# Kernel optimization log

Hardware: AMD Instinct MI355X
Metric: run time of the kernel (lower is better)

Reference implementation:

```python
import jax, jax.numpy as jnp
import numpy as np

TEMPERATURE = 1.0
TOP_K = 50
TOP_P = 0.95
NEG_INF = float('-inf')


def setup_inputs() -> dict:
    key = jax.random.key(0)
    k1, k2, k3, k4 = jax.random.split(key, 4)
    B, S, D, V = 32, 8, 1024, 50257
    psi_real = jax.random.normal(k1, (B, S, D), dtype=jnp.float32)
    psi_imag = jax.random.normal(k2, (B, S, D), dtype=jnp.float32)
    W_real = jax.random.normal(k3, (V, D), dtype=jnp.float32) * 0.02
    W_imag = jax.random.normal(k4, (V, D), dtype=jnp.float32) * 0.02
    bias = jnp.zeros((V,), dtype=jnp.float32)
    return {"psi_real": psi_real, "psi_imag": psi_imag, "W_real": W_real,
            "W_imag": W_imag, "bias": bias}


def _legacy_filter(logits, temperature, top_k, top_p):
    # temperature
    l = logits / max(temperature, 1e-8)
    # top-k: keep values >= k-th largest
    if 0 < top_k < l.shape[-1]:
        topk_vals = jax.lax.top_k(l, top_k)[0]          # [B,S,k]
        threshold = topk_vals[..., -1:]
        l = jnp.where(l < threshold, NEG_INF, l)
    # top-p (nucleus): mask tokens where exclusive cumulative prob >= p
    if top_p < 1.0:
        p = max(top_p, 1e-6)
        order = jnp.argsort(-l, axis=-1)                # descending
        sl = jnp.take_along_axis(l, order, axis=-1)
        sp = jax.nn.softmax(sl, axis=-1)
        cum = jnp.cumsum(sp, axis=-1)
        mask = (cum - sp) >= p                          # exclusive cumsum >= p
        mask = mask.at[..., 0].set(False)               # always keep top token
        sl = jnp.where(mask, NEG_INF, sl)
        inv = jnp.argsort(order, axis=-1)               # scatter back to original order
        l = jnp.take_along_axis(sl, inv, axis=-1)
    return l


def reference(psi_real, psi_imag, W_real, W_imag, bias):
    # logits = proj_real(psi.real) + proj_imag(psi.imag) + bias  -> [B,S,V]
    logits = (jnp.einsum('bsd,vd->bsv', psi_real, W_real)
              + jnp.einsum('bsd,vd->bsv', psi_imag, W_imag) + bias)
    sampling_logits = _legacy_filter(logits, TEMPERATURE, TOP_K, TOP_P)
    probs = jax.nn.softmax(sampling_logits, axis=-1)
    # multinomial(probs, 1) == categorical over filtered logits
    tokens = jax.random.categorical(jax.random.key(42), sampling_logits, axis=-1)
    log_probs = jax.nn.log_softmax(logits, axis=-1)
    return logits, tokens, probs, log_probs
```

## Files before the change

kernel.cpp:

```cpp
#include <hip/hip_runtime.h>
#include <stdint.h>
#include <math.h>

#define MM 256
#define KD 1024
#define K2 2048
#define VV 50257
#define NF4 (VV / 4)
#define ROWQ (NF4 + 1)

static constexpr size_t OUT_TOKENS = (size_t)MM * VV;
static constexpr size_t OUT_PROBS  = OUT_TOKENS + MM;
static constexpr size_t OUT_LOGPR  = OUT_PROBS + (size_t)MM * VV;

#define WS_ABUF_BYTES (2u * 1024u * 1024u)

typedef __attribute__((ext_vector_type(8))) short bf16x8;
typedef __attribute__((ext_vector_type(4))) float f32x4;

__device__ __forceinline__ ushort f2bf(float x) {
  unsigned u = __float_as_uint(x);
  unsigned r = u + 0x7FFFu + ((u >> 16) & 1u);
  return (ushort)(r >> 16);
}
__device__ __forceinline__ float bf2f(ushort h) {
  return __uint_as_float(((unsigned)h) << 16);
}

__device__ __forceinline__ unsigned rotl32(unsigned x, int r) {
  return (x << r) | (x >> (32 - r));
}

__device__ __forceinline__ uint2 threefry2x32(unsigned k0, unsigned k1,
                                              unsigned x0, unsigned x1) {
  unsigned ks[3] = {k0, k1, k0 ^ k1 ^ 0x1BD11BDAu};
  const int rot[8] = {13, 15, 26, 6, 17, 29, 16, 24};
  x0 += ks[0]; x1 += ks[1];
  #pragma unroll
  for (int g = 0; g < 5; ++g) {
    const int base = (g & 1) ? 4 : 0;
    #pragma unroll
    for (int i = 0; i < 4; ++i) {
      x0 += x1;
      x1 = rotl32(x1, rot[base + i]);
      x1 ^= x0;
    }
    x0 += ks[(g + 1) % 3];
    x1 += ks[(g + 2) % 3] + (unsigned)(g + 1);
  }
  return make_uint2(x0, x1);
}

__device__ __forceinline__ float gumbel_at(unsigned flat) {
  uint2 r = threefry2x32(0u, 42u, 0u, flat);
  unsigned w = r.x ^ r.y;
  unsigned fb = (w >> 9) | 0x3F800000u;
  float f = __uint_as_float(fb) - 1.0f;
  const float tiny = 1.1754943508222875e-38f;
  float u = fmaxf(tiny, f + tiny);
  float t1 = (float)log((double)u);
  float t3 = (float)log((double)(-t1));
  return -t3;
}

__global__ __launch_bounds__(256)
void k_prep(const float* __restrict__ psi_r, const float* __restrict__ psi_i,
            ushort* __restrict__ a_buf) {
  int t = blockIdx.x * 256 + threadIdx.x;
  int lane = t & 63;
  int mb = (t >> 6) & 15;
  int s = t >> 10;
  int lr = lane & 15, lg = lane >> 4;
  int m = mb * 16 + lr;
  int kloc = (s & 31) * 32 + lg * 8;
  const float* __restrict__ src = (s < 32) ? psi_r : psi_i;
  float4 v0 = *reinterpret_cast<const float4*>(&src[m * KD + kloc]);
  float4 v1 = *reinterpret_cast<const float4*>(&src[m * KD + kloc + 4]);
  float in[8] = {v0.x, v0.y, v0.z, v0.w, v1.x, v1.y, v1.z, v1.w};
  ushort h[8], l[8];
  #pragma unroll
  for (int j = 0; j < 8; ++j) {
    h[j] = f2bf(in[j]);
    l[j] = f2bf(in[j] - bf2f(h[j]));
  }
  size_t base = ((size_t)(s * 16 + mb) * 2) * 512 + (size_t)lane * 8;
  #pragma unroll
  for (int j = 0; j < 8; ++j) {
    a_buf[base + j] = h[j];
    a_buf[base + 512 + j] = l[j];
  }
}

#define BN 32
#define BK 64
#define GT 512

__global__ __launch_bounds__(GT, 4)
void k_gemm(const uint4* __restrict__ a_buf,
            const float* __restrict__ Wr, const float* __restrict__ Wi,
            const float* __restrict__ bias, float* __restrict__ logits) {
  __shared__ ushort sBh[2][BN * BK];
  __shared__ ushort sBl[2][BN * BK];

  const int tid  = threadIdx.x;
  const int lane = tid & 63;
  const int wid  = tid >> 6;
  const int vb   = blockIdx.x * BN;
  const int lr = lane & 15;
  const int lg = lane >> 4;

  const int brow = tid >> 4;
  const int bc4  = (tid & 15) << 2;
  const int gn   = vb + brow;
  const int eoW  = brow * BK + (bc4 ^ ((brow & 7) << 3));

  f32x4 acc[2][2];
  #pragma unroll
  for (int i = 0; i < 2; ++i)
    #pragma unroll
    for (int j = 0; j < 2; ++j)
      #pragma unroll
      for (int q = 0; q < 4; ++q) acc[i][j][q] = 0.f;

  float4 w = make_float4(0.f, 0.f, 0.f, 0.f);
  if (gn < VV) w = *reinterpret_cast<const float4*>(&Wr[(size_t)gn * KD + bc4]);

  int cur = 0;
  for (int s2 = 0; s2 < K2 / BK; ++s2) {
    uint4 vah[2][2], val[2][2];
    #pragma unroll
    for (int kq = 0; kq < 2; ++kq) {
      #pragma unroll
      for (int mi = 0; mi < 2; ++mi) {
        int chunk2 = (((s2 * 2 + kq) * 16) + wid * 2 + mi) * 2;
        vah[kq][mi] = a_buf[(size_t)chunk2 * 64 + lane];
        val[kq][mi] = a_buf[(size_t)(chunk2 + 1) * 64 + lane];
      }
    }
    {
      float in[4] = {w.x, w.y, w.z, w.w};
      ushort h[4], l[4];
      #pragma unroll
      for (int j = 0; j < 4; ++j) {
        h[j] = f2bf(in[j]);
        l[j] = f2bf(in[j] - bf2f(h[j]));
      }
      *reinterpret_cast<uint2*>(&sBh[cur][eoW]) =
          make_uint2((unsigned)h[0] | ((unsigned)h[1] << 16),
                     (unsigned)h[2] | ((unsigned)h[3] << 16));
      *reinterpret_cast<uint2*>(&sBl[cur][eoW]) =
          make_uint2((unsigned)l[0] | ((unsigned)l[1] << 16),
                     (unsigned)l[2] | ((unsigned)l[3] << 16));
    }
    if (s2 < K2 / BK - 1) {
      int kk = (s2 + 1) * BK;
      const float* __restrict__ Bs = (kk < KD) ? Wr : Wi;
      int ko = kk & (KD - 1);
      if (gn < VV)
        w = *reinterpret_cast<const float4*>(&Bs[(size_t)gn * KD + ko + bc4]);
    }
    __syncthreads();

    #pragma unroll
    for (int kq = 0; kq < 2; ++kq) {
      bf16x8 bh[2], bl[2];
      #pragma unroll
      for (int ni = 0; ni < 2; ++ni) {
        int r = ni * 16 + lr;
        int eoff = r * BK + ((kq * 32 + lg * 8) ^ ((r & 7) << 3));
        bh[ni] = *reinterpret_cast<const bf16x8*>(&sBh[cur][eoff]);
        bl[ni] = *reinterpret_cast<const bf16x8*>(&sBl[cur][eoff]);
      }
      #pragma unroll
      for (int mi = 0; mi < 2; ++mi) {
        bf16x8 ah = *reinterpret_cast<bf16x8*>(&vah[kq][mi]);
        bf16x8 al = *reinterpret_cast<bf16x8*>(&val[kq][mi]);
        #pragma unroll
        for (int ni = 0; ni < 2; ++ni) {
          acc[mi][ni] = __builtin_amdgcn_mfma_f32_16x16x32_bf16(ah, bh[ni], acc[mi][ni], 0, 0, 0);
          acc[mi][ni] = __builtin_amdgcn_mfma_f32_16x16x32_bf16(al, bh[ni], acc[mi][ni], 0, 0, 0);
          acc[mi][ni] = __builtin_amdgcn_mfma_f32_16x16x32_bf16(ah, bl[ni], acc[mi][ni], 0, 0, 0);
        }
      }
    }
    cur ^= 1;
  }

  #pragma unroll
  for (int ni = 0; ni < 2; ++ni) {
    int n = vb + ni * 16 + lr;
    if (n < VV) {
      float b = bias[n];
      #pragma unroll
      for (int mi = 0; mi < 2; ++mi) {
        #pragma unroll
        for (int j = 0; j < 4; ++j) {
          int m = wid * 32 + mi * 16 + lg * 4 + j;
          logits[(size_t)m * VV + n] = acc[mi][ni][j] + b;
        }
      }
    }
  }
}

__device__ __forceinline__ unsigned ordf(float f) {
  unsigned u = __float_as_uint(f);
  return u ^ ((u >> 31) ? 0xFFFFFFFFu : 0x80000000u);
}

__global__ __launch_bounds__(1024)
void k_stats(const float* __restrict__ logits, float* __restrict__ ws4) {
  const int row = blockIdx.x;
  const int tid = threadIdx.x;
  const float* __restrict__ x = logits + (size_t)row * VV;

  __shared__ unsigned hist[4096];
  __shared__ float pm[16], ps[16];

  for (int i = tid; i < 4096; i += 1024) hist[i] = 0u;
  __syncthreads();

  float lm = -INFINITY, ls = 0.f;
  for (int i4 = tid; i4 < NF4; i4 += 1024) {
    float4 v4 = *reinterpret_cast<const float4*>(&x[i4 * 4]);
    float vs[4] = {v4.x, v4.y, v4.z, v4.w};
    #pragma unroll
    for (int j = 0; j < 4; ++j) {
      float v = vs[j];
      atomicAdd(&hist[ordf(v) >> 20], 1u);
      if (v <= lm) {
        ls += expf(v - lm);
      } else {
        ls = ls * expf(lm - v) + 1.f;
        lm = v;
      }
    }
  }
  if (tid == 0) {
    float v = x[VV - 1];
    atomicAdd(&hist[ordf(v) >> 20], 1u);
    if (v <= lm) ls += expf(v - lm);
    else { ls = ls * expf(lm - v) + 1.f; lm = v; }
  }
  #pragma unroll
  for (int off = 32; off; off >>= 1) {
    float om = __shfl_xor(lm, off);
    float os = __shfl_xor(ls, off);
    float M = fmaxf(lm, om);
    ls = ls * expf(lm - M) + os * expf(om - M);
    lm = M;
  }
  if ((tid & 63) == 0) { pm[tid >> 6] = lm; ps[tid >> 6] = ls; }
  __syncthreads();

  if (tid < 64) {
    float m2 = (tid < 16) ? pm[tid] : -3e38f;
    float s2 = (tid < 16) ? ps[tid] : 0.f;
    #pragma unroll
    for (int off = 8; off; off >>= 1) {
      float om = __shfl_xor(m2, off);
      float os = __shfl_xor(s2, off);
      float M = fmaxf(m2, om);
      s2 = s2 * expf(m2 - M) + os * expf(om - M);
      m2 = M;
    }
    unsigned seg = 0;
    #pragma unroll 8
    for (int b = 0; b < 64; ++b) seg += hist[tid * 64 + ((b + tid) & 63)];
    unsigned suf = seg;
    #pragma unroll
    for (int off = 1; off < 64; off <<= 1) {
      unsigned o = __shfl_down(suf, off);
      if (tid + off < 64) suf += o;
    }
    unsigned long long mk = __ballot(suf >= 50u);
    int lstar = 63 - __builtin_clzll(mk);
    unsigned above = (lstar < 63) ? (unsigned)__shfl((int)suf, lstar + 1) : 0u;
    if (tid == 0) {
      unsigned cum = above;
      int bin = lstar * 64;
      for (int b = 63; b >= 0; --b) {
        cum += hist[lstar * 64 + b];
        if (cum >= 50u) { bin = lstar * 64 + b; break; }
      }
      ws4[row * 4 + 0] = m2;
      ws4[row * 4 + 1] = logf(s2);
      ws4[row * 4 + 2] = __uint_as_float((unsigned)bin << 20);
    }
  }
}

__global__ __launch_bounds__(1024)
void k_logprobs(const float* __restrict__ logits, const float* __restrict__ ws4,
                float* __restrict__ logpr) {
  const int totq = MM * ROWQ;
  for (int q = blockIdx.x * blockDim.x + threadIdx.x; q < totq;
       q += gridDim.x * blockDim.x) {
    unsigned row = (unsigned)q / (unsigned)ROWQ;
    unsigned c = (unsigned)q - row * ROWQ;
    float mx = ws4[row * 4 + 0], lz = ws4[row * 4 + 1];
    size_t base = (size_t)row * VV;
    if (c < NF4) {
      size_t idx = base + c * 4;
      float4 v = *reinterpret_cast<const float4*>(&logits[idx]);
      *reinterpret_cast<float4*>(&logpr[idx]) =
          make_float4((v.x - mx) - lz, (v.y - mx) - lz,
                      (v.z - mx) - lz, (v.w - mx) - lz);
    } else {
      size_t idx = base + VV - 1;
      logpr[idx] = (logits[idx] - mx) - lz;
    }
  }
}

#define CAP 1024

__global__ __launch_bounds__(1024)
void k_collect(const float* __restrict__ logits, const float* __restrict__ ws4,
               float* __restrict__ probs, float* __restrict__ tokens) {
  const int row = blockIdx.x;
  const int tid = threadIdx.x;
  const float* __restrict__ x = logits + (size_t)row * VV;

  __shared__ float cv[CAP];
  __shared__ int   ci[CAP];
  __shared__ unsigned s_cnt;
  __shared__ float top_v[50];
  __shared__ int   top_i[50];

  if (tid == 0) s_cnt = 0u;
  __syncthreads();

  const unsigned lo = __float_as_uint(ws4[row * 4 + 2]);
  for (int i4 = tid; i4 < NF4; i4 += 1024) {
    float4 v = *reinterpret_cast<const float4*>(&x[i4 * 4]);
    float vs[4] = {v.x, v.y, v.z, v.w};
    #pragma unroll
    for (int j = 0; j < 4; ++j) {
      if (ordf(vs[j]) >= lo) {
        unsigned pos = atomicAdd(&s_cnt, 1u);
        if (pos < CAP) { cv[pos] = vs[j]; ci[pos] = i4 * 4 + j; }
      }
    }
  }
  if (tid == 0) {
    float v = x[VV - 1];
    if (ordf(v) >= lo) {
      unsigned pos = atomicAdd(&s_cnt, 1u);
      if (pos < CAP) { cv[pos] = v; ci[pos] = VV - 1; }
    }
  }
  __syncthreads();
  const int ncand = (int)min(s_cnt, (unsigned)CAP);

  if (tid < 64) {
    for (int it = 0; it < 50; ++it) {
      float bv = -INFINITY;
      int bi = 0x7FFFFFFF, bs = 0;
      for (int c = tid; c < ncand; c += 64) {
        float v = cv[c];
        int id = ci[c];
        if (v > bv || (v == bv && id < bi)) { bv = v; bi = id; bs = c; }
      }
      #pragma unroll
      for (int off = 32; off; off >>= 1) {
        float ov = __shfl_xor(bv, off);
        int oi = __shfl_xor(bi, off);
        int os = __shfl_xor(bs, off);
        if (ov > bv || (ov == bv && oi < bi)) { bv = ov; bi = oi; bs = os; }
      }
      if (tid == 0) {
        top_v[it] = bv;
        top_i[it] = bi;
        cv[bs] = -INFINITY;
      }
    }

    float tv = (tid < 50) ? top_v[tid] : -3e38f;
    float mx = top_v[0];
    float sp = (tid < 50) ? expf(tv - mx) : 0.f;
    float Z = sp;
    #pragma unroll
    for (int off = 32; off; off >>= 1) Z += __shfl_xor(Z, off);
    float pref = sp;
    #pragma unroll
    for (int off = 1; off < 64; off <<= 1) {
      float o = __shfl_up(pref, off);
      if (tid >= off) pref += o;
    }
    float excl = (pref - sp) / Z;
    bool keep = (tid < 50) && ((tid == 0) || (excl < 0.95f));
    float spk = keep ? sp : 0.f;
    float Z2 = spk;
    #pragma unroll
    for (int off = 32; off; off >>= 1) Z2 += __shfl_xor(Z2, off);

    float bt = -3e38f;
    int bidx = 0x7FFFFFFF;
    if (keep) {
      int idx = top_i[tid];
      probs[(size_t)row * VV + idx] = sp / Z2;
      bt = tv + gumbel_at((unsigned)((size_t)row * VV + idx));
      bidx = idx;
    }
    #pragma unroll
    for (int off = 32; off; off >>= 1) {
      float ot = __shfl_xor(bt, off);
      int oi = __shfl_xor(bidx, off);
      if (ot > bt || (ot == bt && oi < bidx)) { bt = ot; bidx = oi; }
    }
    if (tid == 0) tokens[row] = (float)bidx;
  }
}

extern "C" void kernel_launch(void* const* d_in, const int* in_sizes, int n_in,
                              void* d_out, int out_size, void* d_ws, size_t ws_size,
                              hipStream_t stream) {
  const float* psi_r = (const float*)d_in[0];
  const float* psi_i = (const float*)d_in[1];
  const float* Wr    = (const float*)d_in[2];
  const float* Wi    = (const float*)d_in[3];
  const float* bias  = (const float*)d_in[4];
  float* out = (float*)d_out;

  ushort* a_buf = (ushort*)d_ws;
  float* ws4    = (float*)((char*)d_ws + WS_ABUF_BYTES);

  float* logits = out;
  float* tokens = out + OUT_TOKENS;
  float* probs  = out + OUT_PROBS;
  float* logpr  = out + OUT_LOGPR;

  k_prep<<<256, 256, 0, stream>>>(psi_r, psi_i, a_buf);
  const int nblk = (VV + BN - 1) / BN;
  k_gemm<<<nblk, GT, 0, stream>>>((const uint4*)a_buf, Wr, Wi, bias, logits);
  hipMemsetAsync(probs, 0, (size_t)MM * VV * sizeof(float), stream);
  k_stats<<<MM, 1024, 0, stream>>>(logits, ws4);
  k_logprobs<<<2048, 1024, 0, stream>>>(logits, ws4, logpr);
  k_collect<<<MM, 1024, 0, stream>>>(logits, ws4, probs, tokens);
}
```

Baseline: 350.1 us.

## Widen GEMM N-tile, replicate histogram, fuse probs zeroing into logprobs

The GEMM tile width goes from 32 to 64 vocab columns per block, with each thread loading 8 weights, so the A fragments held in registers are reused across twice as many columns. The __syncthreads is replaced by an explicit lgkmcnt wait plus s_barrier. The stats kernel spreads histogram atomics over four padded replicas to cut LDS contention, then merges them. The separate memset of probs is folded into the logprobs kernel, which now also writes zeros. The costs are higher register pressure in the GEMM, half as many GEMM blocks, and extra LDS use in the stats kernel.

```diff
diff --git a/kernel.cpp b/kernel.cpp
--- a/kernel.cpp
+++ b/kernel.cpp
@@ -91,7 +91,7 @@
   }
 }
 
-#define BN 32
+#define BN 64
 #define BK 64
 #define GT 512
 
@@ -109,21 +109,24 @@
   const int lr = lane & 15;
   const int lg = lane >> 4;
 
-  const int brow = tid >> 4;
-  const int bc4  = (tid & 15) << 2;
+  const int brow = tid >> 3;
+  const int bc8  = (tid & 7) << 3;
   const int gn   = vb + brow;
-  const int eoW  = brow * BK + (bc4 ^ ((brow & 7) << 3));
-
-  f32x4 acc[2][2];
+  const int eoW  = brow * BK + (bc8 ^ ((brow & 7) << 3));
+
+  f32x4 acc[2][4];
   #pragma unroll
   for (int i = 0; i < 2; ++i)
     #pragma unroll
-    for (int j = 0; j < 2; ++j)
+    for (int j = 0; j < 4; ++j)
       #pragma unroll
       for (int q = 0; q < 4; ++q) acc[i][j][q] = 0.f;
 
-  float4 w = make_float4(0.f, 0.f, 0.f, 0.f);
-  if (gn < VV) w = *reinterpret_cast<const float4*>(&Wr[(size_t)gn * KD + bc4]);
+  float4 wa = make_float4(0.f, 0.f, 0.f, 0.f), wb = wa;
+  if (gn < VV) {
+    wa = *reinterpret_cast<const float4*>(&Wr[(size_t)gn * KD + bc8]);
+    wb = *reinterpret_cast<const float4*>(&Wr[(size_t)gn * KD + bc8 + 4]);
+  }
 
   int cur = 0;
   for (int s2 = 0; s2 < K2 / BK; ++s2) {
@@ -138,34 +141,41 @@
       }
     }
     {
-      float in[4] = {w.x, w.y, w.z, w.w};
-      ushort h[4], l[4];
-      #pragma unroll
-      for (int j = 0; j < 4; ++j) {
+      float in[8] = {wa.x, wa.y, wa.z, wa.w, wb.x, wb.y, wb.z, wb.w};
+      ushort h[8], l[8];
+      #pragma unroll
+      for (int j = 0; j < 8; ++j) {
         h[j] = f2bf(in[j]);
         l[j] = f2bf(in[j] - bf2f(h[j]));
       }
-      *reinterpret_cast<uint2*>(&sBh[cur][eoW]) =
-          make_uint2((unsigned)h[0] | ((unsigned)h[1] << 16),
-                     (unsigned)h[2] | ((unsigned)h[3] << 16));
-      *reinterpret_cast<uint2*>(&sBl[cur][eoW]) =
-          make_uint2((unsigned)l[0] | ((unsigned)l[1] << 16),
-                     (unsigned)l[2] | ((unsigned)l[3] << 16));
+      *reinterpret_cast<uint4*>(&sBh[cur][eoW]) =
+          make_uint4((unsigned)h[0] | ((unsigned)h[1] << 16),
+                     (unsigned)h[2] | ((unsigned)h[3] << 16),
+                     (unsigned)h[4] | ((unsigned)h[5] << 16),
+                     (unsigned)h[6] | ((unsigned)h[7] << 16));
+      *reinterpret_cast<uint4*>(&sBl[cur][eoW]) =
+          make_uint4((unsigned)l[0] | ((unsigned)l[1] << 16),
+                     (unsigned)l[2] | ((unsigned)l[3] << 16),
+                     (unsigned)l[4] | ((unsigned)l[5] << 16),
+                     (unsigned)l[6] | ((unsigned)l[7] << 16));
     }
     if (s2 < K2 / BK - 1) {
       int kk = (s2 + 1) * BK;
       const float* __restrict__ Bs = (kk < KD) ? Wr : Wi;
       int ko = kk & (KD - 1);
-      if (gn < VV)
-        w = *reinterpret_cast<const float4*>(&Bs[(size_t)gn * KD + ko + bc4]);
-    }
-    __syncthreads();
+      if (gn < VV) {
+        wa = *reinterpret_cast<const float4*>(&Bs[(size_t)gn * KD + ko + bc8]);
+        wb = *reinterpret_cast<const float4*>(&Bs[(size_t)gn * KD + ko + bc8 + 4]);
+      }
+    }
+    asm volatile("s_waitcnt lgkmcnt(0)" ::: "memory");
+    asm volatile("s_barrier" ::: "memory");
 
     #pragma unroll
     for (int kq = 0; kq < 2; ++kq) {
-      bf16x8 bh[2], bl[2];
-      #pragma unroll
-      for (int ni = 0; ni < 2; ++ni) {
+      bf16x8 bh[4], bl[4];
+      #pragma unroll
+      for (int ni = 0; ni < 4; ++ni) {
         int r = ni * 16 + lr;
         int eoff = r * BK + ((kq * 32 + lg * 8) ^ ((r & 7) << 3));
         bh[ni] = *reinterpret_cast<const bf16x8*>(&sBh[cur][eoff]);
@@ -176,7 +186,7 @@
         bf16x8 ah = *reinterpret_cast<bf16x8*>(&vah[kq][mi]);
         bf16x8 al = *reinterpret_cast<bf16x8*>(&val[kq][mi]);
         #pragma unroll
-        for (int ni = 0; ni < 2; ++ni) {
+        for (int ni = 0; ni < 4; ++ni) {
           acc[mi][ni] = __builtin_amdgcn_mfma_f32_16x16x32_bf16(ah, bh[ni], acc[mi][ni], 0, 0, 0);
           acc[mi][ni] = __builtin_amdgcn_mfma_f32_16x16x32_bf16(al, bh[ni], acc[mi][ni], 0, 0, 0);
           acc[mi][ni] = __builtin_amdgcn_mfma_f32_16x16x32_bf16(ah, bl[ni], acc[mi][ni], 0, 0, 0);
@@ -187,7 +197,7 @@
   }
 
   #pragma unroll
-  for (int ni = 0; ni < 2; ++ni) {
+  for (int ni = 0; ni < 4; ++ni) {
     int n = vb + ni * 16 + lr;
     if (n < VV) {
       float b = bias[n];
@@ -208,18 +218,22 @@
   return u ^ ((u >> 31) ? 0xFFFFFFFFu : 0x80000000u);
 }
 
+#define HREP 4
+#define HSTRIDE 4097
+
 __global__ __launch_bounds__(1024)
 void k_stats(const float* __restrict__ logits, float* __restrict__ ws4) {
   const int row = blockIdx.x;
   const int tid = threadIdx.x;
   const float* __restrict__ x = logits + (size_t)row * VV;
 
-  __shared__ unsigned hist[4096];
+  __shared__ unsigned hist[HREP * HSTRIDE];
   __shared__ float pm[16], ps[16];
 
-  for (int i = tid; i < 4096; i += 1024) hist[i] = 0u;
+  for (int i = tid; i < HREP * HSTRIDE; i += 1024) hist[i] = 0u;
   __syncthreads();
 
+  const int rep = (tid & 3) * HSTRIDE;
   float lm = -INFINITY, ls = 0.f;
   for (int i4 = tid; i4 < NF4; i4 += 1024) {
     float4 v4 = *reinterpret_cast<const float4*>(&x[i4 * 4]);
@@ -227,7 +241,7 @@
     #pragma unroll
     for (int j = 0; j < 4; ++j) {
       float v = vs[j];
-      atomicAdd(&hist[ordf(v) >> 20], 1u);
+      atomicAdd(&hist[rep + (ordf(v) >> 20)], 1u);
       if (v <= lm) {
         ls += expf(v - lm);
       } else {
@@ -251,6 +265,10 @@
     lm = M;
   }
   if ((tid & 63) == 0) { pm[tid >> 6] = lm; ps[tid >> 6] = ls; }
+  __syncthreads();
+
+  for (int b = tid; b < 4096; b += 1024)
+    hist[b] = hist[b] + hist[HSTRIDE + b] + hist[2 * HSTRIDE + b] + hist[3 * HSTRIDE + b];
   __syncthreads();
 
   if (tid < 64) {
@@ -292,7 +310,7 @@
 
 __global__ __launch_bounds__(1024)
 void k_logprobs(const float* __restrict__ logits, const float* __restrict__ ws4,
-                float* __restrict__ logpr) {
+                float* __restrict__ logpr, float* __restrict__ probs) {
   const int totq = MM * ROWQ;
   for (int q = blockIdx.x * blockDim.x + threadIdx.x; q < totq;
        q += gridDim.x * blockDim.x) {
@@ -306,9 +324,11 @@
       *reinterpret_cast<float4*>(&logpr[idx]) =
           make_float4((v.x - mx) - lz, (v.y - mx) - lz,
                       (v.z - mx) - lz, (v.w - mx) - lz);
+      *reinterpret_cast<float4*>(&probs[idx]) = make_float4(0.f, 0.f, 0.f, 0.f);
     } else {
       size_t idx = base + VV - 1;
       logpr[idx] = (logits[idx] - mx) - lz;
+      probs[idx] = 0.f;
     }
   }
 }
@@ -434,8 +454,7 @@
   k_prep<<<256, 256, 0, stream>>>(psi_r, psi_i, a_buf);
   const int nblk = (VV + BN - 1) / BN;
   k_gemm<<<nblk, GT, 0, stream>>>((const uint4*)a_buf, Wr, Wi, bias, logits);
-  hipMemsetAsync(probs, 0, (size_t)MM * VV * sizeof(float), stream);
   k_stats<<<MM, 1024, 0, stream>>>(logits, ws4);
-  k_logprobs<<<2048, 1024, 0, stream>>>(logits, ws4, logpr);
+  k_logprobs<<<2048, 1024, 0, stream>>>(logits, ws4, logpr, probs);
   k_collect<<<MM, 1024, 0, stream>>>(logits, ws4, probs, tokens);
 }
```

Result: faster. 287.9 us (-17.8%).
